# Kernel tuning notes

Measured on AMD Instinct MI355X. Metric: run time of the kernel, lower is better.

The kernel has to match this reference:

```python
import jax, jax.numpy as jnp
import numpy as np
import math

B, S, D, H = 8, 512, 768, 12
DK = D // H
NEG = 1.0e9


def _split_heads(x):
    # [B,S,D] -> [B,H,S,DK]
    b, s, d = x.shape
    return x.reshape(b, s, H, DK).transpose(0, 2, 1, 3)


def setup_inputs() -> dict:
    key = jax.random.key(0)
    ks = jax.random.split(key, 16)
    std = 1.0 / math.sqrt(D)
    query = jax.random.normal(ks[0], (B, S, D), jnp.float32)
    key_t = jax.random.normal(ks[1], (B, S, D), jnp.float32)
    # mask: 0 for valid tokens, -10000 sentinel for padding
    mask = jnp.where(jax.random.bernoulli(ks[2], 0.9, (B, S)), 0.0, -10000.0).astype(jnp.float32)
    # span targets: binary [H,B,S,S]
    span_matrix = jax.random.bernoulli(ks[3], 0.1, (H, B, S, S)).astype(jnp.float32)
    def lin(i):
        W = jax.random.normal(ks[4 + 2 * i], (D, D), jnp.float32) * std
        b = jax.random.normal(ks[5 + 2 * i], (D,), jnp.float32) * std
        return W, b
    Wql, bql = lin(0)
    Wkl, bkl = lin(1)
    Wqr, bqr = lin(2)
    Wkr, bkr = lin(3)
    Wq, bq = lin(4)
    Wk, bk = lin(5)
    return dict(query=query, key=key_t, mask=mask, span_matrix=span_matrix,
                Wql=Wql, bql=bql, Wkl=Wkl, bkl=bkl,
                Wqr=Wqr, bqr=bqr, Wkr=Wkr, bkr=bkr,
                Wq=Wq, bq=bq, Wk=Wk, bk=bk)


def _forward(query, key, mask, span_matrix,
             Wql, bql, Wkl, bkl, Wqr, bqr, Wkr, bkr, Wq, bq, Wk, bk):
    scale = 1.0 / math.sqrt(D)  # note: original scales by sqrt(model_dim), not sqrt(d_k)
    idx = jnp.arange(S)
    lower = idx[None, :] <= idx[:, None]  # [S,S] lower-triangular incl. diag
    left_boundary = jnp.where(lower, 0.0, NEG)   # 1e9 above diagonal
    right_boundary = left_boundary.T             # 1e9 below diagonal

    # left branch
    ql = _split_heads(query @ Wql + bql) * scale
    kl = _split_heads(key @ Wkl + bkl)
    left_scores = jnp.einsum('bhqd,bhkd->bhqk', ql, kl)
    theta_l = jax.nn.softmax(left_scores - left_boundary, axis=-1)

    # right branch
    qr = _split_heads(query @ Wqr + bqr) * scale
    kr = _split_heads(key @ Wkr + bkr)
    right_scores = jnp.einsum('bhqd,bhkd->bhqk', qr, kr)
    theta_r = jax.nn.softmax(right_scores - right_boundary, axis=-1)

    # theta_l @ upperTri == inclusive cumsum over last axis (O(S) instead of O(S^2) matmul)
    soft_Mask_l = jnp.cumsum(theta_l, axis=-1)
    # theta_r @ lowerTri == inclusive reverse cumsum over last axis
    soft_Mask_r = jnp.cumsum(theta_r[..., ::-1], axis=-1)[..., ::-1]
    soft_Mask = soft_Mask_l * soft_Mask_r

    # main attention
    q = _split_heads(query @ Wq + bq) * scale
    k = _split_heads(key @ Wk + bk)
    att_scores = jnp.einsum('bhqd,bhkd->bhqk', q, k)
    row_mask = jnp.where(mask == -10000.0, NEG, mask)  # [B,S]
    att_scores = att_scores - row_mask[:, None, :, None] - row_mask[:, None, None, :]
    p_local_attn = jax.nn.softmax(att_scores * soft_Mask, axis=-1)

    # per-head BCE between sigmoid(attn) and span targets; mean over heads of per-head means
    # == global mean since every head has the same element count
    span = span_matrix.transpose(1, 0, 2, 3)  # [B,H,S,S]
    p_sig = jax.nn.sigmoid(p_local_attn)      # in (0.5, 0.732], logs are safe
    bce = -(span * jnp.log(p_sig) + (1.0 - span) * jnp.log1p(-p_sig))
    span_loss = jnp.mean(bce)
    return p_local_attn, span_loss


def reference(query, key, mask, span_matrix,
              Wql, bql, Wkl, bkl, Wqr, bqr, Wkr, bkr, Wq, bq, Wk, bk):
    return _forward(query, key, mask, span_matrix,
                    Wql, bql, Wkl, bkl, Wqr, bqr, Wkr, bkr, Wq, bq, Wk, bk)
```

## Files before the change

### kernel.cpp

```cpp
#include <hip/hip_runtime.h>
#include <math.h>

#define BB 8
#define SS 512
#define DD 768
#define HH 12
#define DKK 64
#define NTOK (BB*SS)
#define NELEM (25165824ull)
#define NPROJ 3145728
#define WSZ   589824
#define SCALEQ 0.03608439182435161f

typedef unsigned short u16;
typedef short short8 __attribute__((ext_vector_type(8)));
typedef float f32x4 __attribute__((ext_vector_type(4)));
typedef unsigned short u16x4 __attribute__((ext_vector_type(4)));

#define MFMA16 __builtin_amdgcn_mfma_f32_16x16x32_bf16

__device__ inline u16 f32_to_bf16(float f) {
    unsigned int u = __float_as_uint(f);
    unsigned int r = u + 0x7fffu + ((u >> 16) & 1u);
    return (u16)(r >> 16);
}
__device__ inline float bf16_to_f32(u16 h) {
    return __uint_as_float(((unsigned int)h) << 16);
}

__device__ __forceinline__ void gld16(const u16* g, u16* l) {
    __builtin_amdgcn_global_load_lds(
        (const __attribute__((address_space(1))) unsigned int*)g,
        (__attribute__((address_space(3))) unsigned int*)l, 16, 0, 0);
}

__global__ __launch_bounds__(64)
void init_loss_kernel(float* lossp) {
    if (threadIdx.x == 0) *lossp = 0.0f;
}

__global__ __launch_bounds__(256)
void cast_wT(const float* __restrict__ W0, const float* __restrict__ W1,
             const float* __restrict__ W2, const float* __restrict__ W3,
             const float* __restrict__ W4, const float* __restrict__ W5,
             u16* __restrict__ WTh, u16* __restrict__ WTl)
{
    __shared__ float tile[32][33];
    const int z = blockIdx.z;
    const float* W;
    switch (z) {
        case 0: W = W0; break; case 1: W = W1; break; case 2: W = W2; break;
        case 3: W = W3; break; case 4: W = W4; break; default: W = W5; break;
    }
    u16* th = WTh + (size_t)z * WSZ;
    u16* tl = WTl + (size_t)z * WSZ;
    const int t = threadIdx.x;
    const int k0 = blockIdx.y * 32, n0 = blockIdx.x * 32;
    const int rr = t >> 3, c0 = (t & 7) * 4;

    float4 v = *(const float4*)(W + (size_t)(k0 + rr) * DD + n0 + c0);
    tile[rr][c0 + 0] = v.x; tile[rr][c0 + 1] = v.y;
    tile[rr][c0 + 2] = v.z; tile[rr][c0 + 3] = v.w;
    __syncthreads();

    u16x4 hw, lw;
#pragma unroll
    for (int i = 0; i < 4; ++i) {
        float f = tile[c0 + i][rr];
        u16 hi = f32_to_bf16(f);
        hw[i] = hi;
        lw[i] = f32_to_bf16(f - bf16_to_f32(hi));
    }
    size_t o = (size_t)(n0 + rr) * DD + k0 + c0;
    *(u16x4*)&th[o] = hw;
    *(u16x4*)&tl[o] = lw;
}

__global__ __launch_bounds__(256)
void cast_X(const float* __restrict__ query, const float* __restrict__ key,
            u16* __restrict__ Xh, u16* __restrict__ Xl)
{
    const float* src = blockIdx.y ? key : query;
    u16* dh = Xh + (size_t)blockIdx.y * NPROJ;
    u16* dl = Xl + (size_t)blockIdx.y * NPROJ;
    size_t i0 = ((size_t)blockIdx.x * 256 + threadIdx.x) * 8;
    float f[8];
    *(float4*)&f[0] = *(const float4*)(src + i0);
    *(float4*)&f[4] = *(const float4*)(src + i0 + 4);
    short8 h, l;
#pragma unroll
    for (int i = 0; i < 8; ++i) {
        u16 hi = f32_to_bf16(f[i]);
        h[i] = (short)hi;
        l[i] = (short)f32_to_bf16(f[i] - bf16_to_f32(hi));
    }
    *(short8*)&dh[i0] = h;
    *(short8*)&dl[i0] = l;
}

__global__ __launch_bounds__(256)
void proj_gemm_gld(const u16* __restrict__ Xh, const u16* __restrict__ Xl,
                   const u16* __restrict__ WTh, const u16* __restrict__ WTl,
                   const float* __restrict__ b0, const float* __restrict__ b1,
                   const float* __restrict__ b2, const float* __restrict__ b3,
                   const float* __restrict__ b4, const float* __restrict__ b5,
                   u16* __restrict__ Ph, u16* __restrict__ Pl)
{
    __shared__ alignas(16) u16 Ash[128][32];
    __shared__ alignas(16) u16 Asl[128][32];
    __shared__ alignas(16) u16 Bsh[128][32];
    __shared__ alignas(16) u16 Bsl[128][32];

    const int z = blockIdx.z;
    const float* bias;
    switch (z) {
        case 0: bias = b0; break; case 1: bias = b1; break; case 2: bias = b2; break;
        case 3: bias = b3; break; case 4: bias = b4; break; default: bias = b5; break;
    }
    const float scl = (z & 1) ? 1.0f : SCALEQ;
    const u16* Ah_g = Xh + (size_t)(z & 1) * NPROJ;
    const u16* Al_g = Xl + (size_t)(z & 1) * NPROJ;
    const u16* WThz = WTh + (size_t)z * WSZ;
    const u16* WTlz = WTl + (size_t)z * WSZ;
    u16* Ch = Ph + (size_t)z * NPROJ;
    u16* Cl = Pl + (size_t)z * NPROJ;
    const bool wlo = (z < 4);

    const int t = threadIdx.x;
    const int w = t >> 6, l = t & 63, quad = l >> 4, ln = l & 15;
    const int m0 = blockIdx.y * 128, n0 = blockIdx.x * 128;
    const int wm = (w & 1) * 64, wn = (w >> 1) * 64;

    const int srow = w * 16 + (l >> 2);
    const int scol = (l & 3) * 8;
    const u16* gAh = Ah_g + (size_t)(m0 + srow) * DD + scol;
    const u16* gAl = Al_g + (size_t)(m0 + srow) * DD + scol;
    const u16* gBh = WThz + (size_t)(n0 + srow) * DD + scol;
    const u16* gBl = WTlz + (size_t)(n0 + srow) * DD + scol;
    u16* lAh0 = &Ash[w * 16][0];      u16* lAh1 = &Ash[w * 16 + 64][0];
    u16* lAl0 = &Asl[w * 16][0];      u16* lAl1 = &Asl[w * 16 + 64][0];
    u16* lBh0 = &Bsh[w * 16][0];      u16* lBh1 = &Bsh[w * 16 + 64][0];
    u16* lBl0 = &Bsl[w * 16][0];      u16* lBl1 = &Bsl[w * 16 + 64][0];
    const size_t rstep = (size_t)64 * DD;

    f32x4 acc[4][4];
#pragma unroll
    for (int i = 0; i < 4; ++i)
#pragma unroll
        for (int jj = 0; jj < 4; ++jj) acc[i][jj] = (f32x4){0.f, 0.f, 0.f, 0.f};

    for (int k0 = 0; k0 < DD; k0 += 32) {
        gld16(gAh + k0, lAh0);  gld16(gAh + k0 + rstep, lAh1);
        gld16(gAl + k0, lAl0);  gld16(gAl + k0 + rstep, lAl1);
        gld16(gBh + k0, lBh0);  gld16(gBh + k0 + rstep, lBh1);
        gld16(gBl + k0, lBl0);  gld16(gBl + k0 + rstep, lBl1);
        __syncthreads();

        short8 afh[4], afl[4], bfh[4], bfl[4];
#pragma unroll
        for (int mt = 0; mt < 4; ++mt) {
            afh[mt] = *(const short8*)&Ash[wm + mt * 16 + ln][quad * 8];
            afl[mt] = *(const short8*)&Asl[wm + mt * 16 + ln][quad * 8];
        }
#pragma unroll
        for (int nt = 0; nt < 4; ++nt) {
            bfh[nt] = *(const short8*)&Bsh[wn + nt * 16 + ln][quad * 8];
            bfl[nt] = *(const short8*)&Bsl[wn + nt * 16 + ln][quad * 8];
        }
#pragma unroll
        for (int mt = 0; mt < 4; ++mt)
#pragma unroll
            for (int nt = 0; nt < 4; ++nt) {
                acc[mt][nt] = MFMA16(afh[mt], bfh[nt], acc[mt][nt], 0, 0, 0);
                acc[mt][nt] = MFMA16(afh[mt], bfl[nt], acc[mt][nt], 0, 0, 0);
                acc[mt][nt] = MFMA16(afl[mt], bfh[nt], acc[mt][nt], 0, 0, 0);
            }
        __syncthreads();
    }

#pragma unroll
    for (int nt = 0; nt < 4; ++nt) {
        const int n = n0 + wn + nt * 16 + ln;
        const float bv = bias[n];
#pragma unroll
        for (int mt = 0; mt < 4; ++mt) {
            const int mbase = m0 + wm + mt * 16 + quad * 4;
#pragma unroll
            for (int reg = 0; reg < 4; ++reg) {
                float c = (acc[mt][nt][reg] + bv) * scl;
                u16 hi = f32_to_bf16(c);
                size_t o = (size_t)(mbase + reg) * DD + n;
                Ch[o] = hi;
                if (wlo) Cl[o] = f32_to_bf16(c - bf16_to_f32(hi));
            }
        }
    }
}

__global__ __launch_bounds__(256)
void proj_gemm_mfma(const float* __restrict__ query, const float* __restrict__ key,
                    const u16* __restrict__ WTh, const u16* __restrict__ WTl,
                    const float* __restrict__ b0, const float* __restrict__ b1,
                    const float* __restrict__ b2, const float* __restrict__ b3,
                    const float* __restrict__ b4, const float* __restrict__ b5,
                    u16* __restrict__ Ph, u16* __restrict__ Pl)
{
    __shared__ alignas(16) u16 Ash[128][40];
    __shared__ alignas(16) u16 Asl[128][40];
    __shared__ alignas(16) u16 Bsh[128][40];
    __shared__ alignas(16) u16 Bsl[128][40];

    const int z = blockIdx.z;
    const float* X = (z & 1) ? key : query;
    const float* bias;
    switch (z) {
        case 0: bias = b0; break; case 1: bias = b1; break; case 2: bias = b2; break;
        case 3: bias = b3; break; case 4: bias = b4; break; default: bias = b5; break;
    }
    const float scl = (z & 1) ? 1.0f : SCALEQ;
    const u16* WThz = WTh + (size_t)z * WSZ;
    const u16* WTlz = WTl + (size_t)z * WSZ;
    u16* Ch = Ph + (size_t)z * NPROJ;
    u16* Cl = Pl + (size_t)z * NPROJ;
    const bool wlo = (z < 4);

    const int t = threadIdx.x;
    const int w = t >> 6, l = t & 63, quad = l >> 4, ln = l & 15;
    const int m0 = blockIdx.y * 128, n0 = blockIdx.x * 128;
    const int wm = (w & 1) * 64, wn = (w >> 1) * 64;

    const int arow = t >> 1, akoff = (t & 1) * 16;
    const int brow = t >> 1, bkoff = (t & 1) * 16;

    f32x4 acc[4][4];
#pragma unroll
    for (int i = 0; i < 4; ++i)
#pragma unroll
        for (int jj = 0; jj < 4; ++jj) acc[i][jj] = (f32x4){0.f, 0.f, 0.f, 0.f};

    for (int k0 = 0; k0 < DD; k0 += 32) {
        {
            const float* asrc = X + (size_t)(m0 + arow) * DD + k0 + akoff;
            float fa[16];
            *(float4*)&fa[0]  = *(const float4*)(asrc + 0);
            *(float4*)&fa[4]  = *(const float4*)(asrc + 4);
            *(float4*)&fa[8]  = *(const float4*)(asrc + 8);
            *(float4*)&fa[12] = *(const float4*)(asrc + 12);
            short8 h0, h1, l0, l1;
#pragma unroll
            for (int i = 0; i < 8; ++i) {
                u16 hi = f32_to_bf16(fa[i]);
                h0[i] = (short)hi;
                l0[i] = (short)f32_to_bf16(fa[i] - bf16_to_f32(hi));
                u16 hi2 = f32_to_bf16(fa[8 + i]);
                h1[i] = (short)hi2;
                l1[i] = (short)f32_to_bf16(fa[8 + i] - bf16_to_f32(hi2));
            }
            *(short8*)&Ash[arow][akoff]     = h0;
            *(short8*)&Ash[arow][akoff + 8] = h1;
            *(short8*)&Asl[arow][akoff]     = l0;
            *(short8*)&Asl[arow][akoff + 8] = l1;
        }
        {
            const u16* bh = WThz + (size_t)(n0 + brow) * DD + k0 + bkoff;
            const u16* bl = WTlz + (size_t)(n0 + brow) * DD + k0 + bkoff;
            *(uint4*)&Bsh[brow][bkoff]     = *(const uint4*)(bh);
            *(uint4*)&Bsh[brow][bkoff + 8] = *(const uint4*)(bh + 8);
            *(uint4*)&Bsl[brow][bkoff]     = *(const uint4*)(bl);
            *(uint4*)&Bsl[brow][bkoff + 8] = *(const uint4*)(bl + 8);
        }
        __syncthreads();

        short8 afh[4], afl[4], bfh[4], bfl[4];
#pragma unroll
        for (int mt = 0; mt < 4; ++mt) {
            afh[mt] = *(const short8*)&Ash[wm + mt * 16 + ln][quad * 8];
            afl[mt] = *(const short8*)&Asl[wm + mt * 16 + ln][quad * 8];
        }
#pragma unroll
        for (int nt = 0; nt < 4; ++nt) {
            bfh[nt] = *(const short8*)&Bsh[wn + nt * 16 + ln][quad * 8];
            bfl[nt] = *(const short8*)&Bsl[wn + nt * 16 + ln][quad * 8];
        }
#pragma unroll
        for (int mt = 0; mt < 4; ++mt)
#pragma unroll
            for (int nt = 0; nt < 4; ++nt) {
                acc[mt][nt] = MFMA16(afh[mt], bfh[nt], acc[mt][nt], 0, 0, 0);
                acc[mt][nt] = MFMA16(afh[mt], bfl[nt], acc[mt][nt], 0, 0, 0);
                acc[mt][nt] = MFMA16(afl[mt], bfh[nt], acc[mt][nt], 0, 0, 0);
            }
        __syncthreads();
    }

#pragma unroll
    for (int nt = 0; nt < 4; ++nt) {
        const int n = n0 + wn + nt * 16 + ln;
        const float bv = bias[n];
#pragma unroll
        for (int mt = 0; mt < 4; ++mt) {
            const int mbase = m0 + wm + mt * 16 + quad * 4;
#pragma unroll
            for (int reg = 0; reg < 4; ++reg) {
                float c = (acc[mt][nt][reg] + bv) * scl;
                u16 hi = f32_to_bf16(c);
                size_t o = (size_t)(mbase + reg) * DD + n;
                Ch[o] = hi;
                if (wlo) Cl[o] = f32_to_bf16(c - bf16_to_f32(hi));
            }
        }
    }
}

#define CHK 128
__global__ __launch_bounds__(512, 4)
void attn_mfma(const u16* __restrict__ Ph, const u16* __restrict__ Pl,
               const float* __restrict__ mask, const float* __restrict__ span,
               float* __restrict__ outp, float* __restrict__ lossp)
{
    __shared__ alignas(16) u16 Kth[CHK][72];
    __shared__ alignas(16) u16 Ktl[CHK][72];
    __shared__ alignas(16) u16 Qsh[16][72];
    __shared__ alignas(16) u16 Qsl[16][72];
    __shared__ float curb[16][516];
    __shared__ float lred[8];

    const int t = threadIdx.x;
    const int blk = blockIdx.x;
    const int qt = blk & 31;
    const int bh = blk >> 5;
    const int b = bh / HH, h = bh % HH;
    const int w = t >> 6, l = t & 63, quad = l >> 4, ln = l & 15;
    const int r = t >> 5, j = t & 31;
    const int qrow = qt * 16 + r;

    float smbr[16];

    auto compute_scores = [&](const u16* Qh, const u16* Ql,
                              const u16* Kh, const u16* Kl, bool use_lo) {
        __syncthreads();
        if (t < 256) {
            int which = t >> 7, tt = t & 127;
            int row = tt >> 3, co = (tt & 7) * 8;
            if (!which) {
                const u16* src = Qh + (size_t)(b * SS + qt * 16 + row) * DD + h * DKK + co;
                *(uint4*)&Qsh[row][co] = *(const uint4*)src;
            } else if (use_lo) {
                const u16* src = Ql + (size_t)(b * SS + qt * 16 + row) * DD + h * DKK + co;
                *(uint4*)&Qsl[row][co] = *(const uint4*)src;
            }
        }
        __syncthreads();
        short8 ah0 = *(const short8*)&Qsh[ln][quad * 8];
        short8 ah1 = *(const short8*)&Qsh[ln][32 + quad * 8];
        short8 al0 = ah0, al1 = ah1;
        if (use_lo) {
            al0 = *(const short8*)&Qsl[ln][quad * 8];
            al1 = *(const short8*)&Qsl[ln][32 + quad * 8];
        }
        for (int kc = 0; kc < SS / CHK; ++kc) {
            {
                int row = t >> 2, co = (t & 3) * 16;
                const u16* src = Kh + (size_t)(b * SS + kc * CHK + row) * DD + h * DKK + co;
                *(uint4*)&Kth[row][co]     = *(const uint4*)(src);
                *(uint4*)&Kth[row][co + 8] = *(const uint4*)(src + 8);
                if (use_lo) {
                    const u16* src2 = Kl + (size_t)(b * SS + kc * CHK + row) * DD + h * DKK + co;
                    *(uint4*)&Ktl[row][co]     = *(const uint4*)(src2);
                    *(uint4*)&Ktl[row][co + 8] = *(const uint4*)(src2 + 8);
                }
            }
            __syncthreads();
            const int nb = w * 16;
            short8 bh0 = *(const short8*)&Kth[nb + ln][quad * 8];
            short8 bh1 = *(const short8*)&Kth[nb + ln][32 + quad * 8];
            f32x4 acc = (f32x4){0.f, 0.f, 0.f, 0.f};
            acc = MFMA16(ah0, bh0, acc, 0, 0, 0);
            acc = MFMA16(ah1, bh1, acc, 0, 0, 0);
            if (use_lo) {
                short8 bl0 = *(const short8*)&Ktl[nb + ln][quad * 8];
                short8 bl1 = *(const short8*)&Ktl[nb + ln][32 + quad * 8];
                acc = MFMA16(ah0, bl0, acc, 0, 0, 0);
                acc = MFMA16(ah1, bl1, acc, 0, 0, 0);
                acc = MFMA16(al0, bh0, acc, 0, 0, 0);
                acc = MFMA16(al1, bh1, acc, 0, 0, 0);
            }
            const int cbase = kc * CHK + nb + ln;
#pragma unroll
            for (int reg = 0; reg < 4; ++reg)
                curb[quad * 4 + reg][cbase] = acc[reg];
            __syncthreads();
        }
    };

    compute_scores(Ph + 0 * (size_t)NPROJ, Pl + 0 * (size_t)NPROJ,
                   Ph + 1 * (size_t)NPROJ, Pl + 1 * (size_t)NPROJ, true);
    {
        float e[16];
        float mx = -3.0e38f;
#pragma unroll
        for (int u = 0; u < 16; ++u) {
            int c = u * 32 + j;
            float v = curb[r][c];
            if (c <= qrow && v > mx) mx = v;
        }
#pragma unroll
        for (int off = 16; off >= 1; off >>= 1) mx = fmaxf(mx, __shfl_xor(mx, off));
        float sum = 0.0f;
#pragma unroll
        for (int u = 0; u < 16; ++u) {
            int c = u * 32 + j;
            float v = (c <= qrow) ? __expf(curb[r][c] - mx) : 0.0f;
            e[u] = v; sum += v;
        }
#pragma unroll
        for (int off = 16; off >= 1; off >>= 1) sum += __shfl_xor(sum, off);
        float inv = 1.0f / sum;
        float run = 0.0f;
#pragma unroll
        for (int u = 0; u < 16; ++u) {
            float sc = e[u];
#pragma unroll
            for (int off = 1; off < 32; off <<= 1) {
                float ww = __shfl_up(sc, off, 32);
                if (j >= off) sc += ww;
            }
            smbr[u] = (run + sc) * inv;
            run += __shfl(sc, 31, 32);
        }
    }

    compute_scores(Ph + 2 * (size_t)NPROJ, Pl + 2 * (size_t)NPROJ,
                   Ph + 3 * (size_t)NPROJ, Pl + 3 * (size_t)NPROJ, true);
    {
        float e[16];
        float mx = -3.0e38f;
#pragma unroll
        for (int u = 0; u < 16; ++u) {
            int c = u * 32 + j;
            float v = curb[r][c];
            if (c >= qrow && v > mx) mx = v;
        }
#pragma unroll
        for (int off = 16; off >= 1; off >>= 1) mx = fmaxf(mx, __shfl_xor(mx, off));
        float sum = 0.0f;
#pragma unroll
        for (int u = 0; u < 16; ++u) {
            int c = u * 32 + j;
            float v = (c >= qrow) ? __expf(curb[r][c] - mx) : 0.0f;
            e[u] = v; sum += v;
        }
#pragma unroll
        for (int off = 16; off >= 1; off >>= 1) sum += __shfl_xor(sum, off);
        float inv = 1.0f / sum;
        float run = 0.0f;
#pragma unroll
        for (int u = 15; u >= 0; --u) {
            float sc = e[u];
#pragma unroll
            for (int off = 1; off < 32; off <<= 1) {
                float ww = __shfl_down(sc, off, 32);
                if (j + off < 32) sc += ww;
            }
            smbr[u] *= (run + sc) * inv;
            run += __shfl(sc, 0, 32);
        }
    }

    compute_scores(Ph + 4 * (size_t)NPROJ, (const u16*)0,
                   Ph + 5 * (size_t)NPROJ, (const u16*)0, false);
    {
        float mv  = mask[b * SS + qrow];
        float rmq = (mv == -10000.0f) ? 1.0e9f : mv;
        float vb[16];
        float mx = -3.0e38f;
#pragma unroll
        for (int u = 0; u < 16; ++u) {
            int c = u * 32 + j;
            float mk  = mask[b * SS + c];
            float rmk = (mk == -10000.0f) ? 1.0e9f : mk;
            float v = (curb[r][c] - rmq - rmk) * smbr[u];
            vb[u] = v;
            mx = fmaxf(mx, v);
        }
#pragma unroll
        for (int off = 16; off >= 1; off >>= 1) mx = fmaxf(mx, __shfl_xor(mx, off));
        float sum = 0.0f;
#pragma unroll
        for (int u = 0; u < 16; ++u) {
            float ev = __expf(vb[u] - mx);
            vb[u] = ev; sum += ev;
        }
#pragma unroll
        for (int off = 16; off >= 1; off >>= 1) sum += __shfl_xor(sum, off);
        float inv = 1.0f / sum;

        float* orow = outp + (((size_t)(b * HH + h) * SS + qrow)) * SS;
        const float* sprow = span + (((size_t)(h * BB + b) * SS + qrow)) * SS;
        float lsum = 0.0f;
#pragma unroll
        for (int u = 0; u < 16; ++u) {
            int c = u * 32 + j;
            float p = vb[u] * inv;
            orow[c] = p;
            float s = sprow[c];
            lsum += __logf(1.0f + __expf(-p)) + (1.0f - s) * p;
        }
#pragma unroll
        for (int off = 32; off >= 1; off >>= 1) lsum += __shfl_xor(lsum, off);
        if ((t & 63) == 0) lred[t >> 6] = lsum;
        __syncthreads();
        if (t == 0) {
            float tot = 0.0f;
#pragma unroll
            for (int i = 0; i < 8; ++i) tot += lred[i];
            atomicAdd(lossp, tot * (float)(1.0 / 25165824.0));
        }
    }
}

extern "C" void kernel_launch(void* const* d_in, const int* in_sizes, int n_in,
                              void* d_out, int out_size, void* d_ws, size_t ws_size,
                              hipStream_t stream)
{
    const float* query = (const float*)d_in[0];
    const float* key_t = (const float*)d_in[1];
    const float* mask  = (const float*)d_in[2];
    const float* span  = (const float*)d_in[3];
    const float* Wql = (const float*)d_in[4];  const float* bql = (const float*)d_in[5];
    const float* Wkl = (const float*)d_in[6];  const float* bkl = (const float*)d_in[7];
    const float* Wqr = (const float*)d_in[8];  const float* bqr = (const float*)d_in[9];
    const float* Wkr = (const float*)d_in[10]; const float* bkr = (const float*)d_in[11];
    const float* Wq  = (const float*)d_in[12]; const float* bq  = (const float*)d_in[13];
    const float* Wk  = (const float*)d_in[14]; const float* bk  = (const float*)d_in[15];

    float* out = (float*)d_out;
    float* lossp = out + NELEM;

    u16* ws16 = (u16*)d_ws;
    u16* WTh = ws16;
    u16* WTl = WTh + (size_t)6 * WSZ;
    u16* Ph  = WTl + (size_t)6 * WSZ;
    u16* Pl  = Ph + (size_t)6 * NPROJ;
    u16* Xh  = Pl + (size_t)4 * NPROJ;
    u16* Xl  = Xh + (size_t)2 * NPROJ;
    const size_t need_big = ((size_t)12 * WSZ + (size_t)14 * NPROJ) * 2;
    const bool bigws = ws_size >= need_big;

    init_loss_kernel<<<dim3(1), dim3(64), 0, stream>>>(lossp);

    cast_wT<<<dim3(24, 24, 6), dim3(256), 0, stream>>>(
        Wql, Wkl, Wqr, Wkr, Wq, Wk, WTh, WTl);

    if (bigws) {
        cast_X<<<dim3(1536, 2), dim3(256), 0, stream>>>(query, key_t, Xh, Xl);
        proj_gemm_gld<<<dim3(DD / 128, NTOK / 128, 6), dim3(256), 0, stream>>>(
            Xh, Xl, WTh, WTl, bql, bkl, bqr, bkr, bq, bk, Ph, Pl);
    } else {
        proj_gemm_mfma<<<dim3(DD / 128, NTOK / 128, 6), dim3(256), 0, stream>>>(
            query, key_t, WTh, WTl, bql, bkl, bqr, bkr, bq, bk, Ph, Pl);
    }

    attn_mfma<<<dim3(96 * 32), dim3(512), 0, stream>>>(
        Ph, Pl, mask, span, out, lossp);
}
```

Before: 483.7 us.

## Skip low-part loads when unused, vectorize projection stores, drop init kernel and Q LDS staging

The init-loss kernel is folded into cast_wT, which removes one launch. The gld projection GEMM now loads and multiplies the low-part A/B tiles only when the low output is needed, cutting load and MFMA work for the main q/k projections. The MFMA operands are swapped so each lane holds four consecutive output columns, which lets the epilogue write 4-wide vector stores with a float4 bias load instead of scalar strided stores. The attention kernel reads Q fragments straight from global memory, dropping the shared-memory staging and two barriers. Skipping the low parts lowers precision for projections where wlo is false, which is a risk if that path previously fed the low part in.

```diff
diff --git a/kernel.cpp b/kernel.cpp
--- a/kernel.cpp
+++ b/kernel.cpp
@@ -34,18 +34,16 @@
         (__attribute__((address_space(3))) unsigned int*)l, 16, 0, 0);
 }
 
-__global__ __launch_bounds__(64)
-void init_loss_kernel(float* lossp) {
-    if (threadIdx.x == 0) *lossp = 0.0f;
-}
-
 __global__ __launch_bounds__(256)
 void cast_wT(const float* __restrict__ W0, const float* __restrict__ W1,
              const float* __restrict__ W2, const float* __restrict__ W3,
              const float* __restrict__ W4, const float* __restrict__ W5,
-             u16* __restrict__ WTh, u16* __restrict__ WTl)
+             u16* __restrict__ WTh, u16* __restrict__ WTl,
+             float* __restrict__ lossp)
 {
     __shared__ float tile[32][33];
+    if (blockIdx.x == 0 && blockIdx.y == 0 && blockIdx.z == 0 && threadIdx.x == 0)
+        *lossp = 0.0f;
     const int z = blockIdx.z;
     const float* W;
     switch (z) {
@@ -151,48 +149,60 @@
 
     for (int k0 = 0; k0 < DD; k0 += 32) {
         gld16(gAh + k0, lAh0);  gld16(gAh + k0 + rstep, lAh1);
-        gld16(gAl + k0, lAl0);  gld16(gAl + k0 + rstep, lAl1);
         gld16(gBh + k0, lBh0);  gld16(gBh + k0 + rstep, lBh1);
-        gld16(gBl + k0, lBl0);  gld16(gBl + k0 + rstep, lBl1);
+        if (wlo) {
+            gld16(gAl + k0, lAl0);  gld16(gAl + k0 + rstep, lAl1);
+            gld16(gBl + k0, lBl0);  gld16(gBl + k0 + rstep, lBl1);
+        }
         __syncthreads();
 
         short8 afh[4], afl[4], bfh[4], bfl[4];
 #pragma unroll
+        for (int mt = 0; mt < 4; ++mt)
+            afh[mt] = *(const short8*)&Ash[wm + mt * 16 + ln][quad * 8];
+#pragma unroll
+        for (int nt = 0; nt < 4; ++nt)
+            bfh[nt] = *(const short8*)&Bsh[wn + nt * 16 + ln][quad * 8];
+        if (wlo) {
+#pragma unroll
+            for (int mt = 0; mt < 4; ++mt)
+                afl[mt] = *(const short8*)&Asl[wm + mt * 16 + ln][quad * 8];
+#pragma unroll
+            for (int nt = 0; nt < 4; ++nt)
+                bfl[nt] = *(const short8*)&Bsl[wn + nt * 16 + ln][quad * 8];
+        }
+#pragma unroll
+        for (int mt = 0; mt < 4; ++mt)
+#pragma unroll
+            for (int nt = 0; nt < 4; ++nt) {
+                acc[mt][nt] = MFMA16(bfh[nt], afh[mt], acc[mt][nt], 0, 0, 0);
+                if (wlo) {
+                    acc[mt][nt] = MFMA16(bfl[nt], afh[mt], acc[mt][nt], 0, 0, 0);
+                    acc[mt][nt] = MFMA16(bfh[nt], afl[mt], acc[mt][nt], 0, 0, 0);
+                }
+            }
+        __syncthreads();
+    }
+
+#pragma unroll
+    for (int nt = 0; nt < 4; ++nt) {
+        const int nb4 = n0 + wn + nt * 16 + quad * 4;
+        float4 bias4 = *(const float4*)(bias + nb4);
+        float bv[4] = {bias4.x, bias4.y, bias4.z, bias4.w};
+#pragma unroll
         for (int mt = 0; mt < 4; ++mt) {
-            afh[mt] = *(const short8*)&Ash[wm + mt * 16 + ln][quad * 8];
-            afl[mt] = *(const short8*)&Asl[wm + mt * 16 + ln][quad * 8];
-        }
-#pragma unroll
-        for (int nt = 0; nt < 4; ++nt) {
-            bfh[nt] = *(const short8*)&Bsh[wn + nt * 16 + ln][quad * 8];
-            bfl[nt] = *(const short8*)&Bsl[wn + nt * 16 + ln][quad * 8];
-        }
-#pragma unroll
-        for (int mt = 0; mt < 4; ++mt)
-#pragma unroll
-            for (int nt = 0; nt < 4; ++nt) {
-                acc[mt][nt] = MFMA16(afh[mt], bfh[nt], acc[mt][nt], 0, 0, 0);
-                acc[mt][nt] = MFMA16(afh[mt], bfl[nt], acc[mt][nt], 0, 0, 0);
-                acc[mt][nt] = MFMA16(afl[mt], bfh[nt], acc[mt][nt], 0, 0, 0);
-            }
-        __syncthreads();
-    }
-
-#pragma unroll
-    for (int nt = 0; nt < 4; ++nt) {
-        const int n = n0 + wn + nt * 16 + ln;
-        const float bv = bias[n];
-#pragma unroll
-        for (int mt = 0; mt < 4; ++mt) {
-            const int mbase = m0 + wm + mt * 16 + quad * 4;
+            const int m = m0 + wm + mt * 16 + ln;
+            u16x4 hv, lv;
 #pragma unroll
             for (int reg = 0; reg < 4; ++reg) {
-                float c = (acc[mt][nt][reg] + bv) * scl;
+                float c = (acc[mt][nt][reg] + bv[reg]) * scl;
                 u16 hi = f32_to_bf16(c);
-                size_t o = (size_t)(mbase + reg) * DD + n;
-                Ch[o] = hi;
-                if (wlo) Cl[o] = f32_to_bf16(c - bf16_to_f32(hi));
-            }
+                hv[reg] = hi;
+                lv[reg] = f32_to_bf16(c - bf16_to_f32(hi));
+            }
+            size_t o = (size_t)m * DD + nb4;
+            *(u16x4*)&Ch[o] = hv;
+            if (wlo) *(u16x4*)&Cl[o] = lv;
         }
     }
 }
@@ -262,12 +272,12 @@
             *(short8*)&Asl[arow][akoff + 8] = l1;
         }
         {
-            const u16* bh = WThz + (size_t)(n0 + brow) * DD + k0 + bkoff;
-            const u16* bl = WTlz + (size_t)(n0 + brow) * DD + k0 + bkoff;
-            *(uint4*)&Bsh[brow][bkoff]     = *(const uint4*)(bh);
-            *(uint4*)&Bsh[brow][bkoff + 8] = *(const uint4*)(bh + 8);
-            *(uint4*)&Bsl[brow][bkoff]     = *(const uint4*)(bl);
-            *(uint4*)&Bsl[brow][bkoff + 8] = *(const uint4*)(bl + 8);
+            const u16* bhp = WThz + (size_t)(n0 + brow) * DD + k0 + bkoff;
+            const u16* blp = WTlz + (size_t)(n0 + brow) * DD + k0 + bkoff;
+            *(uint4*)&Bsh[brow][bkoff]     = *(const uint4*)(bhp);
+            *(uint4*)&Bsh[brow][bkoff + 8] = *(const uint4*)(bhp + 8);
+            *(uint4*)&Bsl[brow][bkoff]     = *(const uint4*)(blp);
+            *(uint4*)&Bsl[brow][bkoff + 8] = *(const uint4*)(blp + 8);
         }
         __syncthreads();
 
@@ -286,28 +296,32 @@
         for (int mt = 0; mt < 4; ++mt)
 #pragma unroll
             for (int nt = 0; nt < 4; ++nt) {
-                acc[mt][nt] = MFMA16(afh[mt], bfh[nt], acc[mt][nt], 0, 0, 0);
-                acc[mt][nt] = MFMA16(afh[mt], bfl[nt], acc[mt][nt], 0, 0, 0);
-                acc[mt][nt] = MFMA16(afl[mt], bfh[nt], acc[mt][nt], 0, 0, 0);
+                acc[mt][nt] = MFMA16(bfh[nt], afh[mt], acc[mt][nt], 0, 0, 0);
+                acc[mt][nt] = MFMA16(bfl[nt], afh[mt], acc[mt][nt], 0, 0, 0);
+                acc[mt][nt] = MFMA16(bfh[nt], afl[mt], acc[mt][nt], 0, 0, 0);
             }
         __syncthreads();
     }
 
 #pragma unroll
     for (int nt = 0; nt < 4; ++nt) {
-        const int n = n0 + wn + nt * 16 + ln;
-        const float bv = bias[n];
+        const int nb4 = n0 + wn + nt * 16 + quad * 4;
+        float4 bias4 = *(const float4*)(bias + nb4);
+        float bv[4] = {bias4.x, bias4.y, bias4.z, bias4.w};
 #pragma unroll
         for (int mt = 0; mt < 4; ++mt) {
-            const int mbase = m0 + wm + mt * 16 + quad * 4;
+            const int m = m0 + wm + mt * 16 + ln;
+            u16x4 hv, lv;
 #pragma unroll
             for (int reg = 0; reg < 4; ++reg) {
-                float c = (acc[mt][nt][reg] + bv) * scl;
+                float c = (acc[mt][nt][reg] + bv[reg]) * scl;
                 u16 hi = f32_to_bf16(c);
-                size_t o = (size_t)(mbase + reg) * DD + n;
-                Ch[o] = hi;
-                if (wlo) Cl[o] = f32_to_bf16(c - bf16_to_f32(hi));
-            }
+                hv[reg] = hi;
+                lv[reg] = f32_to_bf16(c - bf16_to_f32(hi));
+            }
+            size_t o = (size_t)m * DD + nb4;
+            *(u16x4*)&Ch[o] = hv;
+            if (wlo) *(u16x4*)&Cl[o] = lv;
         }
     }
 }
@@ -320,8 +334,6 @@
 {
     __shared__ alignas(16) u16 Kth[CHK][72];
     __shared__ alignas(16) u16 Ktl[CHK][72];
-    __shared__ alignas(16) u16 Qsh[16][72];
-    __shared__ alignas(16) u16 Qsl[16][72];
     __shared__ float curb[16][516];
     __shared__ float lred[8];
 
@@ -338,25 +350,14 @@
 
     auto compute_scores = [&](const u16* Qh, const u16* Ql,
                               const u16* Kh, const u16* Kl, bool use_lo) {
-        __syncthreads();
-        if (t < 256) {
-            int which = t >> 7, tt = t & 127;
-            int row = tt >> 3, co = (tt & 7) * 8;
-            if (!which) {
-                const u16* src = Qh + (size_t)(b * SS + qt * 16 + row) * DD + h * DKK + co;
-                *(uint4*)&Qsh[row][co] = *(const uint4*)src;
-            } else if (use_lo) {
-                const u16* src = Ql + (size_t)(b * SS + qt * 16 + row) * DD + h * DKK + co;
-                *(uint4*)&Qsl[row][co] = *(const uint4*)src;
-            }
-        }
-        __syncthreads();
-        short8 ah0 = *(const short8*)&Qsh[ln][quad * 8];
-        short8 ah1 = *(const short8*)&Qsh[ln][32 + quad * 8];
+        const u16* qb = Qh + (size_t)(b * SS + qt * 16 + ln) * DD + h * DKK;
+        short8 ah0 = *(const short8*)(qb + quad * 8);
+        short8 ah1 = *(const short8*)(qb + 32 + quad * 8);
         short8 al0 = ah0, al1 = ah1;
         if (use_lo) {
-            al0 = *(const short8*)&Qsl[ln][quad * 8];
-            al1 = *(const short8*)&Qsl[ln][32 + quad * 8];
+            const u16* qb2 = Ql + (size_t)(b * SS + qt * 16 + ln) * DD + h * DKK;
+            al0 = *(const short8*)(qb2 + quad * 8);
+            al1 = *(const short8*)(qb2 + 32 + quad * 8);
         }
         for (int kc = 0; kc < SS / CHK; ++kc) {
             {
@@ -547,10 +548,8 @@
     const size_t need_big = ((size_t)12 * WSZ + (size_t)14 * NPROJ) * 2;
     const bool bigws = ws_size >= need_big;
 
-    init_loss_kernel<<<dim3(1), dim3(64), 0, stream>>>(lossp);
-
     cast_wT<<<dim3(24, 24, 6), dim3(256), 0, stream>>>(
-        Wql, Wkl, Wqr, Wkr, Wq, Wk, WTh, WTl);
+        Wql, Wkl, Wqr, Wkr, Wq, Wk, WTh, WTl, lossp);
 
     if (bigws) {
         cast_X<<<dim3(1536, 2), dim3(256), 0, stream>>>(query, key_t, Xh, Xl);
```

New measurement: 455.7 us. -5.8%, faster.
